# Performance work log

Hardware: AMD Instinct MI355X
Metric: run time of the kernel (lower is better)

The kernel has to match this reference:

```python
import jax, jax.numpy as jnp
import numpy as np

H, W = 40, 128
P = H * W            # image tokens
N = P                # point tokens (matches source where N == Hh*Wh)
C = 128
K = 5                # expand_num
PAD = K // 2
KK = K * K           # 25 neighbors
SPOT = 5             # spot_num
NEG = -1e8


def _l2n(x, axis):
    return x / jnp.clip(jnp.linalg.norm(x, axis=axis, keepdims=True), 1e-12)


def _patches(x, mode, cval=0.0):
    # x: (..., H, W) -> (KK, ..., H, W): KxK sliding windows in F.unfold order
    pw = [(0, 0)] * (x.ndim - 2) + [(PAD, PAD), (PAD, PAD)]
    if mode == 'edge':
        xp = jnp.pad(x, pw, mode='edge')
    else:
        xp = jnp.pad(x, pw, mode='constant', constant_values=cval)
    return jnp.stack([xp[..., i:i + H, j:j + W] for i in range(K) for j in range(K)], 0)


def _knn_idx(pts):
    # (N,3) -> (N,KK) nearest-neighbor indices (self first), as knn_points does
    d2 = jnp.sum((pts[:, None, :] - pts[None, :, :]) ** 2, -1)  # (N,N)
    _, idx = jax.lax.top_k(-d2, KK)
    return idx


def setup_inputs():
    key = jax.random.key(0)
    k1, k2, k3 = jax.random.split(key, 3)
    return {
        'im_feats_h': jax.random.normal(k1, (1, P, C), jnp.float32),
        'pc_feats_h': jax.random.normal(k2, (1, N, C), jnp.float32),
        'points_h': jax.random.normal(k3, (1, N, 3), jnp.float32),
    }


def _forward(imf, pcf, nb):
    # imf: (P,C) image features, pcf: (N,C) point features, nb: (N,KK) point knn
    # --- im_similarity_scores ---
    fmap = imf.T.reshape(C, H, W)
    pat = _patches(fmap, 'edge')                                 # (KK,C,H,W)
    sim = jnp.sum(_l2n(pat, 1) * _l2n(fmap, 0)[None], 1)         # (KK,H,W)
    sim_score = jax.nn.softmax(sim, axis=0)
    # --- pairwise_scores im->pc ---
    s = _l2n(imf, -1) @ _l2n(pcf, -1).T                          # (P,N)
    best_score = s.max(-1).reshape(H, W)
    best_index = s.argmax(-1)                                    # (P,)
    # --- im_select_score ---
    conf = _patches(best_score, 'edge')                          # (KK,H,W)
    idxg = jnp.arange(P).reshape(H, W)
    idx_pat = _patches(idxg, 'const', -1).reshape(KK, P)         # (KK,P)
    select = jnp.where(idx_pat.reshape(KK, H, W) == -1, NEG, sim_score * conf)
    # --- im_seeding ---
    sel = select.at[KK // 2].set(NEG).reshape(KK, P).T           # (P,KK)
    _, tki = jax.lax.top_k(sel, SPOT - 1)
    tki = jnp.concatenate([jnp.full((P, 1), KK // 2, tki.dtype), tki], 1)  # (P,SPOT)
    nb_pix = jnp.clip(jnp.take_along_axis(idx_pat.T, tki, 1), 0, P - 1)
    seed = best_index[nb_pix]                                    # (P,SPOT) pc idx
    # --- im_spoting: expand seeds by point knn, scatter mask, topk-reduce ---
    spot = nb[seed].reshape(P, SPOT * KK)                        # (P,125)
    m = jnp.zeros((P, N), jnp.float32).at[jnp.arange(P)[:, None], spot].set(1.0)
    spot_mask, spot_idx_redu = jax.lax.top_k(m, SPOT * KK)
    # --- pc_similarity_scores ---
    sim_pc = jax.nn.softmax(
        jnp.sum(_l2n(pcf, -1)[:, None] * _l2n(pcf[nb], -1), -1), -1)  # (N,KK)
    # --- pc branch (symmetric, source truncated) ---
    s2 = _l2n(pcf, -1) @ _l2n(imf, -1).T                         # (N,P)
    best_pc_score = s2.max(-1)
    best_pc_idx = s2.argmax(-1)
    select_pc = (sim_pc * best_pc_score[nb]).at[:, 0].set(NEG)   # exclude self
    _, tkp = jax.lax.top_k(select_pc, SPOT - 1)
    tkp = jnp.concatenate([jnp.zeros((N, 1), tkp.dtype), tkp], 1)
    pc_seed = best_pc_idx[jnp.take_along_axis(nb, tkp, 1)]       # (N,SPOT) pixel idx
    # --- pc_spoting: expand seeds in a KxK pixel window ---
    off = jnp.arange(-PAD, PAD + 1)
    r = jnp.clip(pc_seed[..., None, None] // W + off[:, None], 0, H - 1)
    c = jnp.clip(pc_seed[..., None, None] % W + off[None, :], 0, W - 1)
    spot2 = (r * W + c).reshape(N, SPOT * KK)                    # (N,125)
    m2 = jnp.zeros((N, P), jnp.float32).at[jnp.arange(N)[:, None], spot2].set(1.0)
    spot_mask_pc, spot_idx_redu_pc = jax.lax.top_k(m2, SPOT * KK)
    return (select[None], spot_mask[None], spot_idx_redu[None],
            spot_idx_redu_pc[None], spot_mask_pc[None])


def reference(im_feats_h, pc_feats_h, points_h):
    nb = _knn_idx(points_h[0])
    return _forward(im_feats_h[0], pc_feats_h[0], nb)
```

## Files before the change

kernel.cpp:

```cpp
#include <hip/hip_runtime.h>
#include <hip/hip_fp16.h>
#include <float.h>
#include <math.h>

#define HH 40
#define WW 128
#define PP 5120
#define NN 5120
#define CC 128
#define KK 25
#define SPOT 5
#define NEGV -1e8f

#define CSPL 8
#define NSEG 16
#define EPS  1e-4f
#define LOSC 2048.0f
#define BSTR 272
#define RSEGS 16
#define RSEGL (NN / RSEGS)
#define NRMB ((PP + NN) / 4)

typedef _Float16 half8 __attribute__((ext_vector_type(8)));
typedef float f32x4 __attribute__((ext_vector_type(4)));

__global__ __launch_bounds__(256) void k_prep(const float* __restrict__ imf,
                                              const float* __restrict__ pcf,
                                              const float* __restrict__ pts,
                                              float* __restrict__ imn, float* __restrict__ pcn,
                                              __half* __restrict__ imh, __half* __restrict__ iml,
                                              __half* __restrict__ pch, __half* __restrict__ pcl,
                                              int* __restrict__ nb, int* __restrict__ cnt) {
    __shared__ int hist[256];
    __shared__ int wsum2[2][4];
    __shared__ int wsum[4];
    __shared__ int wmin[4];
    __shared__ int s_b, s_need, s_cntLess;
    __shared__ unsigned long long sel[32];
    int t = threadIdx.x;
    int wid = t >> 6, lane = t & 63;

    if (blockIdx.x < NRMB) {
        if (blockIdx.x == 0 && t < 4) cnt[t] = 0;
        int row = blockIdx.x * 4 + wid;
        const float* src; float* dst; __half* dh; __half* dl; int r;
        if (row < PP) { src = imf; dst = imn; dh = imh; dl = iml; r = row; }
        else          { src = pcf; dst = pcn; dh = pch; dl = pcl; r = row - PP; }
        float2 v = *(const float2*)&src[r * CC + lane * 2];
        double ss = (double)v.x * (double)v.x + (double)v.y * (double)v.y;
#pragma unroll
        for (int o = 32; o; o >>= 1) ss += __shfl_xor(ss, o);
        double inv = 1.0 / fmax(sqrt(ss), 1e-12);
        float2 o2 = make_float2((float)((double)v.x * inv), (float)((double)v.y * inv));
        *(float2*)&dst[r * CC + lane * 2] = o2;
        __half hx = __float2half_rn(o2.x), hy = __float2half_rn(o2.y);
        float rx = o2.x - __half2float(hx), ry = o2.y - __half2float(hy);
        __half2 hh; hh.x = hx; hh.y = hy;
        __half2 ll; ll.x = __float2half_rn(rx * LOSC); ll.y = __float2half_rn(ry * LOSC);
        *(__half2*)&dh[r * CC + lane * 2] = hh;
        *(__half2*)&dl[r * CC + lane * 2] = ll;
        return;
    }

    int i = blockIdx.x - NRMB;
    float px = pts[i * 3 + 0], py = pts[i * 3 + 1], pz = pts[i * 3 + 2];

    unsigned k[20];
#pragma unroll
    for (int e = 0; e < 20; ++e) {
        int j = e * 256 + t;
        float dx = __fsub_rn(px, pts[j * 3 + 0]);
        float dy = __fsub_rn(py, pts[j * 3 + 1]);
        float dz = __fsub_rn(pz, pts[j * 3 + 2]);
        float s = __fadd_rn(__fadd_rn(__fmul_rn(dx, dx), __fmul_rn(dy, dy)),
                            __fmul_rn(dz, dz));
        k[e] = __float_as_uint(s);
    }

    int need = KK;
    unsigned bpre = 0;
    for (int bit = 7; bit >= 0; --bit) {
        int c = 0;
        unsigned want = bpre << 1;
#pragma unroll
        for (int e = 0; e < 20; ++e)
            c += ((k[e] >> (24 + bit)) == want);
#pragma unroll
        for (int o = 32; o; o >>= 1) c += __shfl_xor(c, o);
        int par = bit & 1;
        if (lane == 0) wsum2[par][wid] = c;
        __syncthreads();
        int tot = wsum2[par][0] + wsum2[par][1] + wsum2[par][2] + wsum2[par][3];
        if (tot >= need) bpre = want;
        else { bpre = want | 1; need -= tot; }
    }
    unsigned prefix = bpre << 24;

    for (int l = 1; l < 4; ++l) {
        int shift = 24 - 8 * l;
        hist[t] = 0;
        __syncthreads();
        unsigned pmask = 0xFFFFFFFFu << (shift + 8);
#pragma unroll
        for (int e = 0; e < 20; ++e)
            if ((k[e] & pmask) == prefix)
                atomicAdd(&hist[(k[e] >> shift) & 255], 1);
        __syncthreads();
        int v = hist[t], c = v;
#pragma unroll
        for (int o = 1; o < 64; o <<= 1) {
            int u = __shfl_up(c, o);
            if (lane >= o) c += u;
        }
        if (lane == 63) wsum[wid] = c;
        __syncthreads();
        for (int wv = 0; wv < wid; ++wv) c += wsum[wv];
        int cex = c - v;
        if (cex < need && c >= need) { s_b = t; s_need = need - cex; }
        __syncthreads();
        prefix |= ((unsigned)s_b) << shift;
        need = s_need;
        __syncthreads();
    }

    unsigned K = prefix;
    int needK = need;

    if (t == 0) s_cntLess = 0;
    __syncthreads();
#pragma unroll
    for (int e = 0; e < 20; ++e) {
        if (k[e] < K) {
            int slot = atomicAdd(&s_cntLess, 1);
            if (slot < 32)
                sel[slot] = ((unsigned long long)k[e] << 32) | (unsigned)(e * 256 + t);
        }
    }
    __syncthreads();
    int nl = s_cntLess;

    if (t < nl) {
        unsigned long long mine = sel[t];
        int rk = 0;
        for (int s = 0; s < nl; ++s) rk += (sel[s] < mine);
        nb[i * KK + rk] = (int)(mine & 0xFFFFFFFFull);
    }

    unsigned tmask = 0;
#pragma unroll
    for (int e = 0; e < 20; ++e)
        if (k[e] == K) tmask |= 1u << e;

    for (int q = 0; q < needK; ++q) {
        int mi = tmask ? ((__ffs(tmask) - 1) * 256 + t) : 0x7fffffff;
#pragma unroll
        for (int o = 32; o; o >>= 1) mi = min(mi, __shfl_xor(mi, o));
        if (lane == 0) wmin[wid] = mi;
        __syncthreads();
        int g = min(min(wmin[0], wmin[1]), min(wmin[2], wmin[3]));
        if (t == 0) nb[i * KK + nl + q] = g;
        if ((g & 255) == t) tmask &= ~(1u << (g >> 8));
        __syncthreads();
    }
}

__global__ __launch_bounds__(256) void k_rowmax(const __half* __restrict__ imh,
                                                const __half* __restrict__ iml,
                                                const __half* __restrict__ pch,
                                                const __half* __restrict__ pcl,
                                                float* __restrict__ pval,
                                                float* __restrict__ pv2,
                                                int* __restrict__ pidx) {
    const __half* Ah = (blockIdx.z == 0) ? imh : pch;
    const __half* Al = (blockIdx.z == 0) ? iml : pcl;
    const __half* Bh = (blockIdx.z == 0) ? pch : imh;
    const __half* Bl = (blockIdx.z == 0) ? pcl : iml;
    __shared__ char sBh[64 * BSTR];
    __shared__ char sBl[64 * BSTR];

    int t = threadIdx.x;
    int wave = t >> 6, l = t & 63;
    int wrow = wave >> 1, wcol = wave & 1;
    int lg = l >> 4, lc = l & 15;
    int rb = blockIdx.x * 64;
    const int segLen = NN / CSPL;
    int segbase = blockIdx.y * segLen;

    half8 Afh[2][4], Afl[2][4];
#pragma unroll
    for (int rt = 0; rt < 2; ++rt)
#pragma unroll
        for (int ks = 0; ks < 4; ++ks) {
            int row = rb + wrow * 32 + rt * 16 + lc;
            int ho = ks * 32 + lg * 8;
            Afh[rt][ks] = *(const half8*)&Ah[(size_t)row * CC + ho];
            Afl[rt][ks] = *(const half8*)&Al[(size_t)row * CC + ho];
        }

    float v1[2][4], v2[2][4]; int i1[2][4];
#pragma unroll
    for (int rt = 0; rt < 2; ++rt)
#pragma unroll
        for (int rg = 0; rg < 4; ++rg) { v1[rt][rg] = -1e30f; v2[rt][rg] = -1e30f; i1[rt][rg] = 0; }

    for (int ch = 0; ch < segLen; ch += 64) {
#pragma unroll
        for (int q = 0; q < 4; ++q) {
            int u = t + q * 256;
            int row = u >> 4, kb = u & 15;
            *(uint4*)(sBh + row * BSTR + kb * 16) =
                *(const uint4*)&Bh[(size_t)(segbase + ch + row) * CC + kb * 8];
            *(uint4*)(sBl + row * BSTR + kb * 16) =
                *(const uint4*)&Bl[(size_t)(segbase + ch + row) * CC + kb * 8];
        }
        __syncthreads();

        f32x4 aH[2][2], aX[2][2];
#pragma unroll
        for (int rt = 0; rt < 2; ++rt)
#pragma unroll
            for (int ct = 0; ct < 2; ++ct) {
                aH[rt][ct] = (f32x4){0.f, 0.f, 0.f, 0.f};
                aX[rt][ct] = (f32x4){0.f, 0.f, 0.f, 0.f};
            }

#pragma unroll
        for (int ks = 0; ks < 4; ++ks) {
            int kb = ks * 64 + lg * 16;
            half8 bh[2], bl[2];
#pragma unroll
            for (int ct = 0; ct < 2; ++ct) {
                int row = wcol * 32 + ct * 16 + lc;
                int off = row * BSTR + kb;
                bh[ct] = *(const half8*)(sBh + off);
                bl[ct] = *(const half8*)(sBl + off);
            }
#pragma unroll
            for (int rt = 0; rt < 2; ++rt)
#pragma unroll
                for (int ct = 0; ct < 2; ++ct) {
                    aH[rt][ct] = __builtin_amdgcn_mfma_f32_16x16x32_f16(
                        Afh[rt][ks], bh[ct], aH[rt][ct], 0, 0, 0);
                    aX[rt][ct] = __builtin_amdgcn_mfma_f32_16x16x32_f16(
                        Afh[rt][ks], bl[ct], aX[rt][ct], 0, 0, 0);
                    aX[rt][ct] = __builtin_amdgcn_mfma_f32_16x16x32_f16(
                        Afl[rt][ks], bh[ct], aX[rt][ct], 0, 0, 0);
                }
        }

#pragma unroll
        for (int rt = 0; rt < 2; ++rt)
#pragma unroll
            for (int ct = 0; ct < 2; ++ct) {
                int c = segbase + ch + wcol * 32 + ct * 16 + lc;
#pragma unroll
                for (int rg = 0; rg < 4; ++rg) {
                    float v = aH[rt][ct][rg] + aX[rt][ct][rg] * (1.0f / LOSC);
                    bool gt = v > v1[rt][rg];
                    v2[rt][rg] = gt ? v1[rt][rg] : fmaxf(v2[rt][rg], v);
                    i1[rt][rg] = gt ? c : i1[rt][rg];
                    v1[rt][rg] = gt ? v : v1[rt][rg];
                }
            }
        __syncthreads();
    }

#pragma unroll
    for (int rt = 0; rt < 2; ++rt)
#pragma unroll
        for (int rg = 0; rg < 4; ++rg) {
            float a1 = v1[rt][rg], a2 = v2[rt][rg]; int ai = i1[rt][rg];
#pragma unroll
            for (int o = 1; o < 16; o <<= 1) {
                float o1 = __shfl_xor(a1, o);
                float o2v = __shfl_xor(a2, o);
                int   oi = __shfl_xor(ai, o);
                if (o1 > a1) { a2 = fmaxf(a1, o2v); a1 = o1; ai = oi; }
                else         { a2 = fmaxf(a2, o1); }
            }
            if (lc == 0) {
                int seg = blockIdx.y * 2 + wcol;
                size_t o = ((size_t)blockIdx.z * NSEG + seg) * PP
                         + rb + wrow * 32 + rt * 16 + lg * 4 + rg;
                pval[o] = a1; pv2[o] = a2; pidx[o] = ai;
            }
        }
}

__global__ void k_reduce_exact(const float* __restrict__ pval, const float* __restrict__ pv2,
                               const int* __restrict__ pidx,
                               const float* __restrict__ imn, const float* __restrict__ pcn,
                               int* __restrict__ bestI, int* __restrict__ bestPI,
                               double* __restrict__ bestSd, double* __restrict__ bestPSd,
                               int* __restrict__ list2, int* __restrict__ cnt) {
    int wid = threadIdx.x >> 6, lane = threadIdx.x & 63;
    int row = blockIdx.x * 4 + wid;
    int side = (row >= PP) ? 1 : 0;
    int r = side ? (row - PP) : row;
    size_t base = (size_t)side * NSEG * PP + r;

    float v1 = -1e30f, v2 = -1e30f; int i1 = 0x7fffffff;
    if (lane < NSEG) {
        v1 = pval[base + (size_t)lane * PP];
        v2 = pv2[base + (size_t)lane * PP];
        i1 = pidx[base + (size_t)lane * PP];
    }
#pragma unroll
    for (int o = 1; o < 16; o <<= 1) {
        float o1 = __shfl_xor(v1, o);
        float o2v = __shfl_xor(v2, o);
        int   oi = __shfl_xor(i1, o);
        if (o1 > v1) { v2 = fmaxf(v1, o2v); v1 = o1; i1 = oi; }
        else         { v2 = fmaxf(v2, o1); }
    }
    int bi = __shfl(i1, 0);
    float b1 = __shfl(v1, 0), b2 = __shfl(v2, 0);

    const float* A = side ? pcn : imn;
    const float* B = side ? imn : pcn;
    float2 av = *(const float2*)&A[(size_t)r * CC + lane * 2];
    float2 bv = *(const float2*)&B[(size_t)bi * CC + lane * 2];
    double s = (double)av.x * (double)bv.x + (double)av.y * (double)bv.y;
#pragma unroll
    for (int o = 32; o; o >>= 1) s += __shfl_xor(s, o);

    if (lane == 0) {
        if (side == 0) { bestI[r] = bi; bestSd[r] = s; }
        else           { bestPI[r] = bi; bestPSd[r] = s; }
        if (b1 - b2 < EPS) {
            int slot = atomicAdd(&cnt[0], 1);
            list2[slot] = r | (side << 16);
        }
    }
}

__global__ void k_recheck64a(const float* __restrict__ imn, const float* __restrict__ pcn,
                             const int* __restrict__ list2, const int* __restrict__ cnt,
                             double* __restrict__ rqv, int* __restrict__ rqi) {
    __shared__ double ad[CC];
    __shared__ double rv[4];
    __shared__ int    ri[4];
    int seg = blockIdx.x, t = threadIdx.x;
    int wid = t >> 6, lane = t & 63;
    int total = cnt[0];
    for (int e = blockIdx.y; e < total; e += gridDim.y) {
        __syncthreads();
        int ent = list2[e];
        int r = ent & 0xffff, side = ent >> 16;
        const float* Arow = (side == 0 ? imn : pcn) + (size_t)r * CC;
        const float* B    = (side == 0 ? pcn : imn);
        if (t < CC) ad[t] = (double)Arow[t];
        __syncthreads();
        double bv = -1e300; int bi = 0x7fffffff;
        for (int j = seg * RSEGL + t; j < (seg + 1) * RSEGL; j += 256) {
            double s0 = 0.0, s1 = 0.0, s2 = 0.0, s3 = 0.0;
#pragma unroll 8
            for (int c4 = 0; c4 < CC / 4; ++c4) {
                float4 b = *(const float4*)&B[(size_t)j * CC + c4 * 4];
                s0 += ad[c4 * 4 + 0] * (double)b.x;
                s1 += ad[c4 * 4 + 1] * (double)b.y;
                s2 += ad[c4 * 4 + 2] * (double)b.z;
                s3 += ad[c4 * 4 + 3] * (double)b.w;
            }
            double s = (s0 + s1) + (s2 + s3);
            if (s > bv || (s == bv && j < bi)) { bv = s; bi = j; }
        }
#pragma unroll
        for (int o = 32; o; o >>= 1) {
            double ov = __shfl_xor(bv, o); int oi = __shfl_xor(bi, o);
            if (ov > bv || (ov == bv && oi < bi)) { bv = ov; bi = oi; }
        }
        if (lane == 0) { rv[wid] = bv; ri[wid] = bi; }
        __syncthreads();
        if (t == 0) {
            for (int wv = 1; wv < 4; ++wv)
                if (rv[wv] > bv || (rv[wv] == bv && ri[wv] < bi)) { bv = rv[wv]; bi = ri[wv]; }
            rqv[(size_t)e * RSEGS + seg] = bv;
            rqi[(size_t)e * RSEGS + seg] = bi;
        }
        __syncthreads();
    }
}

__global__ void k_recheck64b(const int* __restrict__ list2, const int* __restrict__ cnt,
                             const double* __restrict__ rqv, const int* __restrict__ rqi,
                             double* __restrict__ bestSd, int* __restrict__ bestI,
                             double* __restrict__ bestPSd, int* __restrict__ bestPI) {
    int e = blockIdx.x * 256 + threadIdx.x;
    if (e >= cnt[0]) return;
    double bv = rqv[(size_t)e * RSEGS]; int bi = rqi[(size_t)e * RSEGS];
#pragma unroll 4
    for (int s = 1; s < RSEGS; ++s) {
        double ov = rqv[(size_t)e * RSEGS + s]; int oi = rqi[(size_t)e * RSEGS + s];
        if (ov > bv || (ov == bv && oi < bi)) { bv = ov; bi = oi; }
    }
    int ent = list2[e];
    int r = ent & 0xffff, side = ent >> 16;
    if (side == 0) { bestSd[r] = bv; bestI[r] = bi; }
    else           { bestPSd[r] = bv; bestPI[r] = bi; }
}

__device__ __forceinline__ void compact_bits_par(const unsigned* bits,
                                                 float* __restrict__ sm,
                                                 float* __restrict__ si, int lane) {
    unsigned w0 = bits[lane];
    unsigned w1 = bits[64 + lane];
    unsigned w2 = (lane < 32) ? bits[128 + lane] : 0u;
    int c0 = __popc(w0), c1 = __popc(w1), c2 = __popc(w2);
    int s0 = c0, s1 = c1, s2 = c2;
#pragma unroll
    for (int o = 1; o < 64; o <<= 1) {
        int u0 = __shfl_up(s0, o); if (lane >= o) s0 += u0;
        int u1 = __shfl_up(s1, o); if (lane >= o) s1 += u1;
        int u2 = __shfl_up(s2, o); if (lane >= o) s2 += u2;
    }
    int tot0 = __shfl(s0, 63);
    int tot1 = __shfl(s1, 63);
    int tot2 = __shfl(s2, 31);
    int nl = tot0 + tot1 + tot2;
    int e0 = s0 - c0;
    int e1 = tot0 + (s1 - c1);
    int e2 = tot0 + tot1 + (s2 - c2);

    {
        int base = e0; unsigned word = w0; int wi = lane;
        while (word) { int pos = __ffs(word) - 1;
            si[base] = (float)(wi * 32 + pos); sm[base] = 1.0f; word &= word - 1; ++base; }
        base = e1; word = w1; wi = 64 + lane;
        while (word) { int pos = __ffs(word) - 1;
            si[base] = (float)(wi * 32 + pos); sm[base] = 1.0f; word &= word - 1; ++base; }
        if (lane < 32) {
            base = e2; word = w2; wi = 128 + lane;
            while (word) { int pos = __ffs(word) - 1;
                si[base] = (float)(wi * 32 + pos); sm[base] = 1.0f; word &= word - 1; ++base; }
        }
    }
    {
        int wi = lane; int base = nl + 32 * wi - e0; unsigned word = ~w0;
        while (word && base < 125) { int pos = __ffs(word) - 1;
            si[base] = (float)(wi * 32 + pos); sm[base] = 0.0f; word &= word - 1; ++base; }
        wi = 64 + lane; base = nl + 32 * wi - e1; word = ~w1;
        while (word && base < 125) { int pos = __ffs(word) - 1;
            si[base] = (float)(wi * 32 + pos); sm[base] = 0.0f; word &= word - 1; ++base; }
        if (lane < 32) {
            wi = 128 + lane; base = nl + 32 * wi - e2; word = ~w2;
            while (word && base < 125) { int pos = __ffs(word) - 1;
                si[base] = (float)(wi * 32 + pos); sm[base] = 0.0f; word &= word - 1; ++base; }
        }
    }
}

__global__ void k_select_spot(const float* __restrict__ imn, const float* __restrict__ pcn,
                              const int* __restrict__ nb,
                              const double* __restrict__ bestSd, const int* __restrict__ bestI,
                              const double* __restrict__ bestPSd, const int* __restrict__ bestPI,
                              float* __restrict__ outSelect,
                              float* __restrict__ outMask, float* __restrict__ outIdx,
                              float* __restrict__ outMaskPc, float* __restrict__ outIdxPc) {
    __shared__ unsigned bits[4][160];
    __shared__ float smv[4][125];
    __shared__ float siv[4][125];
    int t = threadIdx.x;
    int wid = t >> 6, lane = t & 63;
    int bid = blockIdx.x;

    if (bid < PP / 4) {
        int pb = (bid & 7) * (PP / 4 / 8) + (bid >> 3);
        int p = pb * 4 + wid;
        int h = p >> 7, w = p & 127;

        double mysim = -1e300;
        if (lane < KK) {
            int di = lane / 5 - 2, dj = lane % 5 - 2;
            int hc = min(max(h + di, 0), HH - 1);
            int wc = min(max(w + dj, 0), WW - 1);
            const float* crow = &imn[(size_t)p * CC];
            const float* nrow = &imn[(size_t)(hc * WW + wc) * CC];
            double s0 = 0.0, s1 = 0.0, s2 = 0.0, s3 = 0.0;
#pragma unroll 8
            for (int c = 0; c < CC; c += 4) {
                float4 cv = *(const float4*)&crow[c];
                float4 nv = *(const float4*)&nrow[c];
                s0 += (double)cv.x * (double)nv.x;
                s1 += (double)cv.y * (double)nv.y;
                s2 += (double)cv.z * (double)nv.z;
                s3 += (double)cv.w * (double)nv.w;
            }
            mysim = (s0 + s1) + (s2 + s3);
        }
        double mx = mysim;
#pragma unroll
        for (int o = 1; o < 64; o <<= 1) mx = fmax(mx, __shfl_xor(mx, o));

        double e = 0.0;
        if (lane < KK) e = exp(mysim - mx);
        double sum = e;
#pragma unroll
        for (int o = 32; o; o >>= 1) sum += __shfl_xor(sum, o);
        double inv = 1.0 / sum;

        double selv = -1e300;
        if (lane < KK) {
            int di = lane / 5 - 2, dj = lane % 5 - 2;
            int h2 = h + di, w2 = w + dj;
            bool valid = (h2 >= 0 && h2 < HH && w2 >= 0 && w2 < WW);
            int hc = min(max(h2, 0), HH - 1), wc = min(max(w2, 0), WW - 1);
            double conf = bestSd[hc * WW + wc];
            double so = valid ? (e * inv * conf) : (double)NEGV;
            outSelect[lane * PP + p] = (float)so;
            selv = (lane == 12) ? (double)NEGV : so;
        }

        int tks[5]; tks[0] = 12;
        double sv = selv; int sk = (lane < KK) ? lane : 63;
#pragma unroll
        for (int s = 0; s < 4; ++s) {
            double bv = sv; int bk = sk;
#pragma unroll
            for (int o = 1; o < 64; o <<= 1) {
                double ov = __shfl_xor(bv, o);
                int ok = __shfl_xor(bk, o);
                if (ov > bv || (ov == bv && ok < bk)) { bv = ov; bk = ok; }
            }
            tks[s + 1] = bk;
            if (sk == bk) sv = -1e300;
        }

        int sd0, sd1, sd2, sd3, sd4;
#pragma unroll
        for (int s = 0; s < 5; ++s) {
            int k = tks[s];
            int di = k / 5 - 2, dj = k % 5 - 2;
            int h2 = h + di, w2 = w + dj;
            int pix = (h2 >= 0 && h2 < HH && w2 >= 0 && w2 < WW) ? (h2 * WW + w2) : -1;
            pix = min(max(pix, 0), PP - 1);
            int sd = bestI[pix];
            if (s == 0) sd0 = sd; else if (s == 1) sd1 = sd;
            else if (s == 2) sd2 = sd; else if (s == 3) sd3 = sd; else sd4 = sd;
        }

        for (int w2 = lane; w2 < 160; w2 += 64) bits[wid][w2] = 0u;
        __syncthreads();
        for (int e2 = lane; e2 < 125; e2 += 64) {
            int q = e2 / 25;
            int sd = (q == 0) ? sd0 : (q == 1) ? sd1 : (q == 2) ? sd2 : (q == 3) ? sd3 : sd4;
            int pt = nb[sd * KK + (e2 % 25)];
            atomicOr(&bits[wid][pt >> 5], 1u << (pt & 31));
        }
        __syncthreads();
        compact_bits_par(bits[wid], smv[wid], siv[wid], lane);
        for (int e2 = lane; e2 < 125; e2 += 64) {
            outMask[p * 125 + e2] = smv[wid][e2];
            outIdx[p * 125 + e2]  = siv[wid][e2];
        }
    } else {
        int bid2 = bid - PP / 4;
        int ib = (bid2 & 7) * (PP / 4 / 8) + (bid2 >> 3);
        int i = ib * 4 + wid;

        double mysim = -1e300;
        if (lane < KK) {
            int nbs = nb[i * KK + lane];
            const float* crow = &pcn[(size_t)i * CC];
            const float* nrow = &pcn[(size_t)nbs * CC];
            double s0 = 0.0, s1 = 0.0, s2 = 0.0, s3 = 0.0;
#pragma unroll 8
            for (int c = 0; c < CC; c += 4) {
                float4 cv = *(const float4*)&crow[c];
                float4 nv = *(const float4*)&nrow[c];
                s0 += (double)cv.x * (double)nv.x;
                s1 += (double)cv.y * (double)nv.y;
                s2 += (double)cv.z * (double)nv.z;
                s3 += (double)cv.w * (double)nv.w;
            }
            mysim = (s0 + s1) + (s2 + s3);
        }
        double mx = mysim;
#pragma unroll
        for (int o = 1; o < 64; o <<= 1) mx = fmax(mx, __shfl_xor(mx, o));

        double e = 0.0;
        if (lane < KK) e = exp(mysim - mx);
        double sum = e;
#pragma unroll
        for (int o = 32; o; o >>= 1) sum += __shfl_xor(sum, o);
        double inv = 1.0 / sum;

        double selv = -1e300;
        if (lane < KK)
            selv = (lane == 0) ? (double)NEGV : (e * inv * bestPSd[nb[i * KK + lane]]);

        int tks[5]; tks[0] = 0;
        double sv = selv; int sk = (lane < KK) ? lane : 63;
#pragma unroll
        for (int s = 0; s < 4; ++s) {
            double bv = sv; int bk = sk;
#pragma unroll
            for (int o = 1; o < 64; o <<= 1) {
                double ov = __shfl_xor(bv, o);
                int ok = __shfl_xor(bk, o);
                if (ov > bv || (ov == bv && ok < bk)) { bv = ov; bk = ok; }
            }
            tks[s + 1] = bk;
            if (sk == bk) sv = -1e300;
        }

        int sd0, sd1, sd2, sd3, sd4;
#pragma unroll
        for (int s = 0; s < 5; ++s) {
            int nbs = nb[i * KK + tks[s]];
            int sd = bestPI[nbs];
            if (s == 0) sd0 = sd; else if (s == 1) sd1 = sd;
            else if (s == 2) sd2 = sd; else if (s == 3) sd3 = sd; else sd4 = sd;
        }

        for (int w2 = lane; w2 < 160; w2 += 64) bits[wid][w2] = 0u;
        __syncthreads();
        for (int e2 = lane; e2 < 125; e2 += 64) {
            int q = e2 / 25;
            int sd = (q == 0) ? sd0 : (q == 1) ? sd1 : (q == 2) ? sd2 : (q == 3) ? sd3 : sd4;
            int kk = e2 % 25;
            int r0 = sd >> 7, c0 = sd & 127;
            int r = min(max(r0 + kk / 5 - 2, 0), HH - 1);
            int c = min(max(c0 + kk % 5 - 2, 0), WW - 1);
            int pix = r * WW + c;
            atomicOr(&bits[wid][pix >> 5], 1u << (pix & 31));
        }
        __syncthreads();
        compact_bits_par(bits[wid], smv[wid], siv[wid], lane);
        for (int e2 = lane; e2 < 125; e2 += 64) {
            outMaskPc[i * 125 + e2] = smv[wid][e2];
            outIdxPc[i * 125 + e2]  = siv[wid][e2];
        }
    }
}

extern "C" void kernel_launch(void* const* d_in, const int* in_sizes, int n_in,
                              void* d_out, int out_size, void* d_ws, size_t ws_size,
                              hipStream_t stream) {
    const float* imf = (const float*)d_in[0];
    const float* pcf = (const float*)d_in[1];
    const float* pts = (const float*)d_in[2];
    float* out = (float*)d_out;

    char* w = (char*)d_ws;
    double* bestSd  = (double*)w;  w += (size_t)PP * 8;
    double* bestPSd = (double*)w;  w += (size_t)NN * 8;
    double* rqv     = (double*)w;  w += (size_t)(PP + NN) * RSEGS * 8;
    float*  imn     = (float*)w;   w += (size_t)PP * CC * 4;
    float*  pcn     = (float*)w;   w += (size_t)NN * CC * 4;
    __half* imh     = (__half*)w;  w += (size_t)PP * CC * 2;
    __half* iml     = (__half*)w;  w += (size_t)PP * CC * 2;
    __half* pch     = (__half*)w;  w += (size_t)NN * CC * 2;
    __half* pcl     = (__half*)w;  w += (size_t)NN * CC * 2;
    float*  pval    = (float*)w;   w += (size_t)2 * NSEG * PP * 4;
    float*  pv2     = (float*)w;   w += (size_t)2 * NSEG * PP * 4;
    int*    pidx    = (int*)w;     w += (size_t)2 * NSEG * PP * 4;
    int*    rqi     = (int*)w;     w += (size_t)(PP + NN) * RSEGS * 4;
    int*    nb      = (int*)w;     w += (size_t)NN * KK * 4;
    int*    bestI   = (int*)w;     w += (size_t)PP * 4;
    int*    bestPI  = (int*)w;     w += (size_t)NN * 4;
    int*    list2   = (int*)w;     w += (size_t)(PP + NN) * 4;
    int*    cnt     = (int*)w;     w += 256;

    float* outSelect = out;
    float* outMask   = out + KK * PP;
    float* outIdx    = outMask + PP * 125;
    float* outIdxPc  = outIdx + PP * 125;
    float* outMaskPc = outIdxPc + NN * 125;

    k_prep<<<NRMB + NN, 256, 0, stream>>>(imf, pcf, pts, imn, pcn,
                                          imh, iml, pch, pcl, nb, cnt);
    k_rowmax<<<dim3(PP / 64, CSPL, 2), 256, 0, stream>>>(imh, iml, pch, pcl,
                                                         pval, pv2, pidx);
    k_reduce_exact<<<(PP + NN) / 4, 256, 0, stream>>>(pval, pv2, pidx, imn, pcn,
                                                      bestI, bestPI, bestSd, bestPSd,
                                                      list2, cnt);
    k_recheck64a<<<dim3(RSEGS, 256), 256, 0, stream>>>(imn, pcn, list2, cnt, rqv, rqi);
    k_recheck64b<<<(PP + NN) / 256, 256, 0, stream>>>(list2, cnt, rqv, rqi,
                                                      bestSd, bestI, bestPSd, bestPI);
    k_select_spot<<<2 * PP / 4, 256, 0, stream>>>(imn, pcn, nb, bestSd, bestI,
                                                  bestPSd, bestPI, outSelect,
                                                  outMask, outIdx, outMaskPc, outIdxPc);
}
```

Before: 178.0 us.

## Double-buffer B tiles via direct global-to-LDS loads with XOR swizzle

Reworks B-tile staging in the rowmax GEMM kernel. Tiles now load straight from global memory into LDS with global_load_lds, into two ping-pong buffers, so the next chunk's fetch overlaps the current chunk's MFMA work. The padded stride layout is replaced by an XOR swizzle to avoid LDS bank conflicts. This doubles LDS use to 64KB per block, which may lower occupancy. The loop now has a single barrier per iteration, and correctness relies on the direct-to-LDS loads having completed by that barrier.

Result: no change. 175.3 us (-1.5%).

```diff
diff --git a/kernel.cpp b/kernel.cpp
--- a/kernel.cpp
+++ b/kernel.cpp
@@ -16,7 +16,6 @@
 #define NSEG 16
 #define EPS  1e-4f
 #define LOSC 2048.0f
-#define BSTR 272
 #define RSEGS 16
 #define RSEGL (NN / RSEGS)
 #define NRMB ((PP + NN) / 4)
@@ -175,8 +174,7 @@
     const __half* Al = (blockIdx.z == 0) ? iml : pcl;
     const __half* Bh = (blockIdx.z == 0) ? pch : imh;
     const __half* Bl = (blockIdx.z == 0) ? pcl : iml;
-    __shared__ char sBh[64 * BSTR];
-    __shared__ char sBl[64 * BSTR];
+    __shared__ char sB[2 * 32768];
 
     int t = threadIdx.x;
     int wave = t >> 6, l = t & 63;
@@ -184,7 +182,10 @@
     int lg = l >> 4, lc = l & 15;
     int rb = blockIdx.x * 64;
     const int segLen = NN / CSPL;
+    const int nCh = segLen / 64;
     int segbase = blockIdx.y * segLen;
+    int srow = l >> 4;
+    int sblk = l & 15;
 
     half8 Afh[2][4], Afl[2][4];
 #pragma unroll
@@ -203,17 +204,33 @@
 #pragma unroll
         for (int rg = 0; rg < 4; ++rg) { v1[rt][rg] = -1e30f; v2[rt][rg] = -1e30f; i1[rt][rg] = 0; }
 
-    for (int ch = 0; ch < segLen; ch += 64) {
-#pragma unroll
-        for (int q = 0; q < 4; ++q) {
-            int u = t + q * 256;
-            int row = u >> 4, kb = u & 15;
-            *(uint4*)(sBh + row * BSTR + kb * 16) =
-                *(const uint4*)&Bh[(size_t)(segbase + ch + row) * CC + kb * 8];
-            *(uint4*)(sBl + row * BSTR + kb * 16) =
-                *(const uint4*)&Bl[(size_t)(segbase + ch + row) * CC + kb * 8];
-        }
-        __syncthreads();
+    auto stage = [&](int bufsel, int chbase) {
+#pragma unroll
+        for (int b = 0; b < 4; ++b) {
+            int rbase = wave * 16 + b * 4;
+            int r = rbase + srow;
+            int gblk = sblk ^ (r & 7);
+            __builtin_amdgcn_global_load_lds(
+                (const __attribute__((address_space(1))) void*)
+                    &Bh[(size_t)(chbase + r) * CC + gblk * 8],
+                (__attribute__((address_space(3))) void*)
+                    (sB + bufsel * 32768 + rbase * 256),
+                16, 0, 0);
+            __builtin_amdgcn_global_load_lds(
+                (const __attribute__((address_space(1))) void*)
+                    &Bl[(size_t)(chbase + r) * CC + gblk * 8],
+                (__attribute__((address_space(3))) void*)
+                    (sB + bufsel * 32768 + 16384 + rbase * 256),
+                16, 0, 0);
+        }
+    };
+
+    stage(0, segbase);
+    __syncthreads();
+
+    int cur = 0;
+    for (int c = 0; c < nCh; ++c) {
+        if (c + 1 < nCh) stage(cur ^ 1, segbase + (c + 1) * 64);
 
         f32x4 aH[2][2], aX[2][2];
 #pragma unroll
@@ -224,6 +241,7 @@
                 aX[rt][ct] = (f32x4){0.f, 0.f, 0.f, 0.f};
             }
 
+        const char* bufp = sB + cur * 32768;
 #pragma unroll
         for (int ks = 0; ks < 4; ++ks) {
             int kb = ks * 64 + lg * 16;
@@ -231,9 +249,9 @@
 #pragma unroll
             for (int ct = 0; ct < 2; ++ct) {
                 int row = wcol * 32 + ct * 16 + lc;
-                int off = row * BSTR + kb;
-                bh[ct] = *(const half8*)(sBh + off);
-                bl[ct] = *(const half8*)(sBl + off);
+                int off = row * 256 + (kb ^ ((row & 7) << 4));
+                bh[ct] = *(const half8*)(bufp + off);
+                bl[ct] = *(const half8*)(bufp + 16384 + off);
             }
 #pragma unroll
             for (int rt = 0; rt < 2; ++rt)
@@ -252,17 +270,18 @@
         for (int rt = 0; rt < 2; ++rt)
 #pragma unroll
             for (int ct = 0; ct < 2; ++ct) {
-                int c = segbase + ch + wcol * 32 + ct * 16 + lc;
+                int col = segbase + c * 64 + wcol * 32 + ct * 16 + lc;
 #pragma unroll
                 for (int rg = 0; rg < 4; ++rg) {
                     float v = aH[rt][ct][rg] + aX[rt][ct][rg] * (1.0f / LOSC);
                     bool gt = v > v1[rt][rg];
                     v2[rt][rg] = gt ? v1[rt][rg] : fmaxf(v2[rt][rg], v);
-                    i1[rt][rg] = gt ? c : i1[rt][rg];
+                    i1[rt][rg] = gt ? col : i1[rt][rg];
                     v1[rt][rg] = gt ? v : v1[rt][rg];
                 }
             }
         __syncthreads();
+        cur ^= 1;
     }
 
 #pragma unroll
```
